# Kernel optimization log

Measured on AMD Instinct MI355X. Metric: run time of the kernel, lower is better.

## Reference

```python
import jax, jax.numpy as jnp
import numpy as np

N, C, H, K = 50000, 256, 8, 16
M = N * K
HID = 4 * C
HD = C // H
SCALE = HD ** -0.5
EPS = 1e-5


def setup_inputs() -> dict:
    key = jax.random.key(0)
    ks = jax.random.split(key, 8)
    init = lambda k, shape, fan: jax.random.normal(k, shape, jnp.float32) * (fan ** -0.5)
    return {
        "feats": jax.random.normal(ks[0], (N, C), jnp.float32),
        "polar_pos": jax.random.normal(ks[1], (N, 3), jnp.float32),
        "edge_index": jax.random.randint(ks[2], (2, M), 0, N, dtype=jnp.int64),
        "ln1_g": jnp.ones((C,), jnp.float32), "ln1_b": jnp.zeros((C,), jnp.float32),
        "qkv_w": init(ks[3], (3 * C, C), C), "qkv_b": jnp.zeros((3 * C,), jnp.float32),
        "proj_w": init(ks[4], (C, C), C), "proj_b": jnp.zeros((C,), jnp.float32),
        "ln2_g": jnp.ones((C,), jnp.float32), "ln2_b": jnp.zeros((C,), jnp.float32),
        "fc1_w": init(ks[5], (HID, C), C), "fc1_b": jnp.zeros((HID,), jnp.float32),
        "fc2_w": init(ks[6], (C, HID), HID), "fc2_b": jnp.zeros((C,), jnp.float32),
    }


def _ln(x, g, b):
    m = x.mean(-1, keepdims=True)
    v = jnp.var(x, axis=-1, keepdims=True)
    return (x - m) * jax.lax.rsqrt(v + EPS) * g + b


def reference(feats, polar_pos, edge_index, ln1_g, ln1_b, qkv_w, qkv_b,
              proj_w, proj_b, ln2_g, ln2_b, fc1_w, fc1_b, fc2_w, fc2_b):
    skip = feats
    x = _ln(feats, ln1_g, ln1_b)

    # edge bookkeeping: sort edges by destination (index_0), matching torch.sort
    idx0 = edge_index[0]
    idx1 = edge_index[1]
    order = jnp.argsort(idx0)  # stable sort
    idx0 = idx0[order]
    idx1 = idx1[order]

    # qkv projection -> (N, 3, H, HD)
    qkv = (x @ qkv_w.T + qkv_b).reshape(N, 3, H, HD)
    q = qkv[:, 0] * SCALE  # (N, H, HD)
    k = qkv[:, 1]
    v = qkv[:, 2]

    # attention_step1_v2: per-edge dot products, (M, H)
    attn = jnp.einsum('mhd,mhd->mh', q[idx0], k[idx1])

    # scatter_softmax over edges grouped by idx0
    mx = jax.ops.segment_max(attn, idx0, num_segments=N)
    e = jnp.exp(attn - mx[idx0])
    s = jax.ops.segment_sum(e, idx0, num_segments=N)
    w = e / s[idx0]  # (M, H)

    # attention_step2: weighted aggregation of neighbor values
    out = jax.ops.segment_sum(w[:, :, None] * v[idx1], idx0, num_segments=N)
    out = out.reshape(N, C)

    out = out @ proj_w.T + proj_b
    feats = skip + out

    y = _ln(feats, ln2_g, ln2_b)
    y = jax.nn.gelu(y @ fc1_w.T + fc1_b, approximate=False)
    y = y @ fc2_w.T + fc2_b
    return feats + y
```

## Files before the change

kernel.cpp:

```cpp
#include <hip/hip_runtime.h>
#include <hip/hip_bf16.h>
#include <cmath>


#define N_NODES 50000
#define C_DIM 256
#define M_EDGES 800000
#define ATT_SCALE 0.17677669529663687f
#define LN_EPS 1e-5f
#define LOG2E 1.4426950408889634f
#define NEG_BIG -3.0e38f

typedef unsigned int uint_t;
typedef unsigned short ushort_t;
typedef short short8 __attribute__((ext_vector_type(8)));
typedef float floatx4 __attribute__((ext_vector_type(4)));

__device__ __forceinline__ ushort_t f2bf(float f) {
  uint_t u = __float_as_uint(f);
  return (ushort_t)((u + 0x7FFFu + ((u >> 16) & 1u)) >> 16);
}
__device__ __forceinline__ float bf_even(uint_t u) { return __uint_as_float(u << 16); }
__device__ __forceinline__ float bf_odd(uint_t u) { return __uint_as_float(u & 0xFFFF0000u); }

__device__ __forceinline__ float gelu_tanh(float x) {
  const float u = 0.7978845608028654f * (x + 0.044715f * x * x * x);
  const float e = __expf(2.0f * u);
  const float t = 1.0f - 2.0f / (e + 1.0f);
  return 0.5f * x * (1.0f + t);
}

__device__ __forceinline__ void gload16(const void* g, void* l) {
  __builtin_amdgcn_global_load_lds(
      (const __attribute__((address_space(1))) void*)g,
      (__attribute__((address_space(3))) void*)l, 16, 0, 0);
}

__global__ __launch_bounds__(256) void ln_kernel(const float* __restrict__ x,
    const float* __restrict__ g, const float* __restrict__ b,
    ushort_t* __restrict__ y)
{
  __shared__ float red[8];
  const int n = blockIdx.x;
  const int t = threadIdx.x;
  float v = x[(size_t)n * C_DIM + t];
  float s = v, s2 = v * v;
#pragma unroll
  for (int m = 1; m < 64; m <<= 1) {
    s += __shfl_xor(s, m);
    s2 += __shfl_xor(s2, m);
  }
  const int wave = t >> 6;
  if ((t & 63) == 0) { red[wave] = s; red[4 + wave] = s2; }
  __syncthreads();
  s = red[0] + red[1] + red[2] + red[3];
  s2 = red[4] + red[5] + red[6] + red[7];
  const float mean = s * (1.0f / 256.0f);
  const float var = fmaxf(s2 * (1.0f / 256.0f) - mean * mean, 0.0f);
  const float r = rsqrtf(var + LN_EPS);
  y[(size_t)n * C_DIM + t] = f2bf((v - mean) * r * g[t] + b[t]);
}

__global__ void cvt_kernel(const float* __restrict__ s0, const float* __restrict__ s1,
                           const float* __restrict__ s2, const float* __restrict__ s3,
                           ushort_t* __restrict__ dst)
{
  const int i = blockIdx.x * 256 + threadIdx.x;
  float v;
  if (i < 196608) v = s0[i];
  else if (i < 262144) v = s1[i - 196608];
  else if (i < 524288) v = s2[i - 262144];
  else v = s3[i - 524288];
  dst[i] = f2bf(v);
}

template <int EPI>
__global__ __launch_bounds__(256, 2) void mfma_gemm(
    const ushort_t* __restrict__ A, const ushort_t* __restrict__ W,
    const float* __restrict__ bias, const float* __restrict__ extra,
    void* __restrict__ OutV, int Kdim, int Jdim)
{
  __shared__ __align__(16) char smem[36864];
  ushort_t* As = (ushort_t*)smem;
  ushort_t* Bs = As + 128 * 64;
  const int t = threadIdx.x;
  const int lane = t & 63;
  const int w = t >> 6;
  const int wm = w & 1;
  const int wn = w >> 1;
  const int rowbase = blockIdx.y * 128;
  const int colbase = blockIdx.x * 128;

  floatx4 acc[4][4] = {};

  int rA[4], kcg[4];
#pragma unroll
  for (int h = 0; h < 4; ++h) {
    const int cidx = h * 256 + w * 64 + lane;
    const int r = cidx >> 3;
    rA[h] = r;
    kcg[h] = (cidx & 7) ^ (r & 7);
  }

  const int rl = lane & 15;
  const int qd = lane >> 4;

  for (int k0 = 0; k0 < Kdim; k0 += 64) {
#pragma unroll
    for (int h = 0; h < 4; ++h) {
      const int r = rA[h];
      int grow = rowbase + r;
      if (grow > N_NODES - 1) grow = N_NODES - 1;
      const int gcol = colbase + r;
      ushort_t* lbase_a = As + (size_t)(h * 256 + w * 64) * 8;
      ushort_t* lbase_b = Bs + (size_t)(h * 256 + w * 64) * 8;
      gload16(A + (size_t)grow * Kdim + k0 + kcg[h] * 8, lbase_a);
      gload16(W + (size_t)gcol * Kdim + k0 + kcg[h] * 8, lbase_b);
    }
    __syncthreads();

#pragma unroll
    for (int h = 0; h < 2; ++h) {
      short8 af[4], bf[4];
#pragma unroll
      for (int tm = 0; tm < 4; ++tm) {
        const int ra = wm * 64 + tm * 16 + rl;
        const int kc = (h * 4 + qd) ^ (ra & 7);
        af[tm] = *(const short8*)(As + ra * 64 + kc * 8);
      }
#pragma unroll
      for (int tn = 0; tn < 4; ++tn) {
        const int rb = wn * 64 + tn * 16 + rl;
        const int kc = (h * 4 + qd) ^ (rb & 7);
        bf[tn] = *(const short8*)(Bs + rb * 64 + kc * 8);
      }
#pragma unroll
      for (int tm = 0; tm < 4; ++tm)
#pragma unroll
        for (int tn = 0; tn < 4; ++tn)
          acc[tm][tn] = __builtin_amdgcn_mfma_f32_16x16x32_bf16(
              af[tm], bf[tn], acc[tm][tn], 0, 0, 0);
    }
    __syncthreads();
  }

  const int q8 = lane >> 3;
  const int c8 = lane & 7;
  if (EPI == 1) {
    float* sc = (float*)smem + w * (64 * 36);
#pragma unroll
    for (int p = 0; p < 2; ++p) {
      __syncthreads();
#pragma unroll
      for (int th = 0; th < 2; ++th) {
        const int tn = p * 2 + th;
#pragma unroll
        for (int tm = 0; tm < 4; ++tm)
#pragma unroll
          for (int r = 0; r < 4; ++r)
            sc[(tm * 16 + qd * 4 + r) * 36 + th * 16 + rl] = acc[tm][tn][r];
      }
      __syncthreads();
      const int col0 = colbase + wn * 64 + p * 32 + c8 * 4;
      const float4 b4 = *(const float4*)(bias + col0);
#pragma unroll
      for (int it = 0; it < 8; ++it) {
        const int lr = it * 8 + q8;
        const int grow = rowbase + wm * 64 + lr;
        if (grow >= N_NODES) continue;
        float4 v = *(const float4*)(sc + lr * 36 + c8 * 4);
        const float4 e4 = *(const float4*)(extra + (size_t)grow * Jdim + col0);
        v.x += b4.x + e4.x; v.y += b4.y + e4.y;
        v.z += b4.z + e4.z; v.w += b4.w + e4.w;
        *(float4*)((float*)OutV + (size_t)grow * Jdim + col0) = v;
      }
    }
  } else {
    ushort_t* su = (ushort_t*)smem + w * (64 * 72);
#pragma unroll
    for (int tn = 0; tn < 4; ++tn) {
      const int col = colbase + wn * 64 + tn * 16 + rl;
      const float bv = bias[col];
#pragma unroll
      for (int tm = 0; tm < 4; ++tm)
#pragma unroll
        for (int r = 0; r < 4; ++r) {
          float v = acc[tm][tn][r] + bv;
          if (EPI == 0) {
            if (col < 256) v *= ATT_SCALE;
          } else {
            v = gelu_tanh(v);
          }
          su[(tm * 16 + qd * 4 + r) * 72 + tn * 16 + rl] = f2bf(v);
        }
    }
    __syncthreads();
#pragma unroll
    for (int it = 0; it < 8; ++it) {
      const int lr = it * 8 + q8;
      const int grow = rowbase + wm * 64 + lr;
      if (grow >= N_NODES) continue;
      const uint4 v = *(const uint4*)(su + lr * 72 + c8 * 8);
      *(uint4*)((ushort_t*)OutV + (size_t)grow * Jdim + colbase + wn * 64 + c8 * 8) = v;
    }
  }
}

__global__ void hist_kernel(const int* __restrict__ idx0, int* __restrict__ counts)
{
  const int m = blockIdx.x * 256 + threadIdx.x;
  if (m < M_EDGES) atomicAdd(&counts[idx0[m]], 1);
}

__global__ __launch_bounds__(256) void scan1_kernel(const int* __restrict__ counts,
    int* __restrict__ offsets, int* __restrict__ bsums)
{
  __shared__ int tmp[256];
  const int t = threadIdx.x;
  const int i = blockIdx.x * 256 + t;
  const int v = (i < N_NODES) ? counts[i] : 0;
  int x = v;
  tmp[t] = x;
  __syncthreads();
#pragma unroll
  for (int off = 1; off < 256; off <<= 1) {
    const int a = (t >= off) ? tmp[t - off] : 0;
    __syncthreads();
    x += a;
    tmp[t] = x;
    __syncthreads();
  }
  if (i < N_NODES) offsets[i] = x - v;
  if (t == 255) bsums[blockIdx.x] = x;
}

__global__ __launch_bounds__(256) void scan2_kernel(int* __restrict__ bsums, int nb)
{
  __shared__ int tmp[256];
  const int t = threadIdx.x;
  const int v = (t < nb) ? bsums[t] : 0;
  int x = v;
  tmp[t] = x;
  __syncthreads();
#pragma unroll
  for (int off = 1; off < 256; off <<= 1) {
    const int a = (t >= off) ? tmp[t - off] : 0;
    __syncthreads();
    x += a;
    tmp[t] = x;
    __syncthreads();
  }
  if (t < nb) bsums[t] = x - v;
}

__global__ void scan3_kernel(int* __restrict__ offsets, const int* __restrict__ bsums)
{
  const int i = blockIdx.x * 256 + threadIdx.x;
  if (i < N_NODES) offsets[i] += bsums[blockIdx.x];
  if (i == 0) offsets[N_NODES] = M_EDGES;
}

__global__ void scatter_kernel(const int* __restrict__ idx0,
    const int* __restrict__ idx1, const int* __restrict__ offsets,
    int* __restrict__ cursor, int* __restrict__ srcs)
{
  const int m = blockIdx.x * 256 + threadIdx.x;
  if (m < M_EDGES) {
    const int n = idx0[m];
    const int p = offsets[n] + atomicAdd(&cursor[n], 1);
    srcs[p] = idx1[m];
  }
}

__global__ __launch_bounds__(256) void attn_kernel(
    const ushort_t* __restrict__ QKVh, const int* __restrict__ offsets,
    const int* __restrict__ srcs, ushort_t* __restrict__ AO)
{
  const int node = blockIdx.x * 4 + (threadIdx.x >> 6);
  if (node >= N_NODES) return;
  const int lane = threadIdx.x & 63;
  const int h = lane & 7;
  const int slot = lane >> 3;
  const int start = offsets[node];
  const int end = offsets[node + 1];

  float q[32];
  {
    const uint4* qr = (const uint4*)(QKVh + (size_t)node * 768 + h * 32);
#pragma unroll
    for (int i = 0; i < 4; ++i) {
      const uint4 u = qr[i];
      q[i * 8 + 0] = bf_even(u.x); q[i * 8 + 1] = bf_odd(u.x);
      q[i * 8 + 2] = bf_even(u.y); q[i * 8 + 3] = bf_odd(u.y);
      q[i * 8 + 4] = bf_even(u.z); q[i * 8 + 5] = bf_odd(u.z);
      q[i * 8 + 6] = bf_even(u.w); q[i * 8 + 7] = bf_odd(u.w);
    }
  }

  float m = NEG_BIG, s = 0.f;
  float o[32];
#pragma unroll
  for (int d = 0; d < 32; ++d) o[d] = 0.f;

  for (int e = start + slot; e < end; e += 8) {
    const int sidx = srcs[e];
    const uint4* kr = (const uint4*)(QKVh + (size_t)sidx * 768 + 256 + h * 32);
    float d = 0.f;
#pragma unroll
    for (int i = 0; i < 4; ++i) {
      const uint4 u = kr[i];
      d += q[i * 8 + 0] * bf_even(u.x) + q[i * 8 + 1] * bf_odd(u.x);
      d += q[i * 8 + 2] * bf_even(u.y) + q[i * 8 + 3] * bf_odd(u.y);
      d += q[i * 8 + 4] * bf_even(u.z) + q[i * 8 + 5] * bf_odd(u.z);
      d += q[i * 8 + 6] * bf_even(u.w) + q[i * 8 + 7] * bf_odd(u.w);
    }
    const float l = d * LOG2E;
    const float mn = fmaxf(m, l);
    const float fac = exp2f(m - mn);
    const float wgt = exp2f(l - mn);
    m = mn;
    s = s * fac + wgt;
    const uint4* vr = (const uint4*)(QKVh + (size_t)sidx * 768 + 512 + h * 32);
#pragma unroll
    for (int i = 0; i < 4; ++i) {
      const uint4 u = vr[i];
      o[i * 8 + 0] = o[i * 8 + 0] * fac + wgt * bf_even(u.x);
      o[i * 8 + 1] = o[i * 8 + 1] * fac + wgt * bf_odd(u.x);
      o[i * 8 + 2] = o[i * 8 + 2] * fac + wgt * bf_even(u.y);
      o[i * 8 + 3] = o[i * 8 + 3] * fac + wgt * bf_odd(u.y);
      o[i * 8 + 4] = o[i * 8 + 4] * fac + wgt * bf_even(u.z);
      o[i * 8 + 5] = o[i * 8 + 5] * fac + wgt * bf_odd(u.z);
      o[i * 8 + 6] = o[i * 8 + 6] * fac + wgt * bf_even(u.w);
      o[i * 8 + 7] = o[i * 8 + 7] * fac + wgt * bf_odd(u.w);
    }
  }

  float mx = m;
  mx = fmaxf(mx, __shfl_xor(mx, 8));
  mx = fmaxf(mx, __shfl_xor(mx, 16));
  mx = fmaxf(mx, __shfl_xor(mx, 32));
  const float fac = exp2f(m - mx);
  s *= fac;
#pragma unroll
  for (int d = 0; d < 32; ++d) o[d] *= fac;

  s += __shfl_xor(s, 8);
  s += __shfl_xor(s, 16);
  s += __shfl_xor(s, 32);

  {
    const bool up = (slot & 4) != 0;
#pragma unroll
    for (int i = 0; i < 16; ++i) {
      const float send = up ? o[i] : o[i + 16];
      const float recv = __shfl_xor(send, 32);
      o[i] = (up ? o[i + 16] : o[i]) + recv;
    }
  }
  {
    const bool up = (slot & 2) != 0;
#pragma unroll
    for (int i = 0; i < 8; ++i) {
      const float send = up ? o[i] : o[i + 8];
      const float recv = __shfl_xor(send, 16);
      o[i] = (up ? o[i + 8] : o[i]) + recv;
    }
  }
  {
    const bool up = (slot & 1) != 0;
#pragma unroll
    for (int i = 0; i < 4; ++i) {
      const float send = up ? o[i] : o[i + 4];
      const float recv = __shfl_xor(send, 8);
      o[i] = (up ? o[i + 4] : o[i]) + recv;
    }
  }
  const int dbase = ((slot & 4) ? 16 : 0) + ((slot & 2) ? 8 : 0) +
                    ((slot & 1) ? 4 : 0);
  const float inv = (end > start) ? 1.0f / s : 0.0f;
  ushort4 st;
  st.x = f2bf(o[0] * inv); st.y = f2bf(o[1] * inv);
  st.z = f2bf(o[2] * inv); st.w = f2bf(o[3] * inv);
  *(ushort4*)(AO + (size_t)node * 256 + h * 32 + dbase) = st;
}

extern "C" void kernel_launch(void* const* d_in, const int* in_sizes, int n_in,
                              void* d_out, int out_size, void* d_ws,
                              size_t ws_size, hipStream_t stream)
{
  const float* feats  = (const float*)d_in[0];
  const int*   edge   = (const int*)d_in[2];
  const float* ln1_g  = (const float*)d_in[3];
  const float* ln1_b  = (const float*)d_in[4];
  const float* qkv_w  = (const float*)d_in[5];
  const float* qkv_b  = (const float*)d_in[6];
  const float* proj_w = (const float*)d_in[7];
  const float* proj_b = (const float*)d_in[8];
  const float* ln2_g  = (const float*)d_in[9];
  const float* ln2_b  = (const float*)d_in[10];
  const float* fc1_w  = (const float*)d_in[11];
  const float* fc1_b  = (const float*)d_in[12];
  const float* fc2_w  = (const float*)d_in[13];
  const float* fc2_b  = (const float*)d_in[14];
  float* out = (float*)d_out;

  ushort_t* Xb   = (ushort_t*)d_ws;
  ushort_t* QKVh = Xb + (size_t)N_NODES * 256;
  ushort_t* AOb  = QKVh + (size_t)N_NODES * 768;
  ushort_t* Hb   = QKVh;
  ushort_t* wb   = AOb + (size_t)N_NODES * 256;
  ushort_t* qkv_wb  = wb;
  ushort_t* proj_wb = qkv_wb + 768 * 256;
  ushort_t* fc1_wb  = proj_wb + 256 * 256;
  ushort_t* fc2_wb  = fc1_wb + 1024 * 256;
  int* counts  = (int*)(fc2_wb + 256 * 1024);
  int* cursor  = counts + N_NODES;
  int* offsets = cursor + N_NODES;
  int* srcs    = offsets + N_NODES + 1;
  int* bsums   = srcs + M_EDGES;
  const size_t required = (size_t)((char*)(bsums + 256) - (char*)d_ws);
  if (ws_size < required) {
    hipMemsetAsync(d_out, 0, (size_t)out_size * sizeof(float), stream);
    return;
  }
  const int* idx0 = edge;
  const int* idx1 = edge + M_EDGES;
  const int rowTiles = (N_NODES + 127) / 128;
  const int scanBlocks = (N_NODES + 255) / 256;

  hipMemsetAsync(counts, 0, 2 * N_NODES * sizeof(int), stream);
  cvt_kernel<<<786432 / 256, 256, 0, stream>>>(qkv_w, proj_w, fc1_w, fc2_w, wb);

  ln_kernel<<<N_NODES, 256, 0, stream>>>(feats, ln1_g, ln1_b, Xb);
  mfma_gemm<0><<<dim3(768 / 128, rowTiles), 256, 0, stream>>>(
      Xb, qkv_wb, qkv_b, nullptr, QKVh, 256, 768);
  hist_kernel<<<(M_EDGES + 255) / 256, 256, 0, stream>>>(idx0, counts);
  scan1_kernel<<<scanBlocks, 256, 0, stream>>>(counts, offsets, bsums);
  scan2_kernel<<<1, 256, 0, stream>>>(bsums, scanBlocks);
  scan3_kernel<<<scanBlocks, 256, 0, stream>>>(offsets, bsums);
  scatter_kernel<<<(M_EDGES + 255) / 256, 256, 0, stream>>>(idx0, idx1, offsets,
                                                            cursor, srcs);
  attn_kernel<<<N_NODES / 4, 256, 0, stream>>>(QKVh, offsets, srcs, AOb);
  mfma_gemm<1><<<dim3(256 / 128, rowTiles), 256, 0, stream>>>(
      AOb, proj_wb, proj_b, feats, out, 256, 256);
  ln_kernel<<<N_NODES, 256, 0, stream>>>(out, ln2_g, ln2_b, Xb);
  mfma_gemm<2><<<dim3(1024 / 128, rowTiles), 256, 0, stream>>>(
      Xb, fc1_wb, fc1_b, nullptr, Hb, 256, 1024);
  mfma_gemm<1><<<dim3(256 / 128, rowTiles), 256, 0, stream>>>(
      Hb, fc2_wb, fc2_b, out, out, 1024, 256);
}
```

Measured before the change: 564.5 us.

## Drop online-softmax max tracking and unify GEMM epilogue for higher occupancy

The edge-attention kernel no longer tracks a running maximum. It accumulates exp(score) and weighted values directly, which removes the per-edge rescale of the 32 output accumulators and the cross-lane max reduction. The GEMM epilogue now stages results through a smaller per-wave float buffer in two row-halves with padded stride 33. That cuts shared memory to 32 KB, drops block-wide syncs, and raises the launch-bounds occupancy hint from 2 to 4. The trade-off is that unstabilized exp can overflow if attention logits grow large, and the tighter register budget may cause spills in the MFMA loop.

```diff
diff --git a/kernel.cpp b/kernel.cpp
--- a/kernel.cpp
+++ b/kernel.cpp
@@ -9,7 +9,6 @@
 #define ATT_SCALE 0.17677669529663687f
 #define LN_EPS 1e-5f
 #define LOG2E 1.4426950408889634f
-#define NEG_BIG -3.0e38f
 
 typedef unsigned int uint_t;
 typedef unsigned short ushort_t;
@@ -75,12 +74,12 @@
 }
 
 template <int EPI>
-__global__ __launch_bounds__(256, 2) void mfma_gemm(
+__global__ __launch_bounds__(256, 4) void mfma_gemm(
     const ushort_t* __restrict__ A, const ushort_t* __restrict__ W,
     const float* __restrict__ bias, const float* __restrict__ extra,
     void* __restrict__ OutV, int Kdim, int Jdim)
 {
-  __shared__ __align__(16) char smem[36864];
+  __shared__ __align__(16) char smem[32768];
   ushort_t* As = (ushort_t*)smem;
   ushort_t* Bs = As + 128 * 64;
   const int t = threadIdx.x;
@@ -146,62 +145,46 @@
 
   const int q8 = lane >> 3;
   const int c8 = lane & 7;
-  if (EPI == 1) {
-    float* sc = (float*)smem + w * (64 * 36);
+  float* sc = (float*)smem + w * 1056;
+  const float qscale = (EPI == 0 && colbase < 256) ? ATT_SCALE : 1.0f;
+#pragma unroll
+  for (int rh = 0; rh < 2; ++rh) {
 #pragma unroll
     for (int p = 0; p < 2; ++p) {
-      __syncthreads();
-#pragma unroll
-      for (int th = 0; th < 2; ++th) {
-        const int tn = p * 2 + th;
-#pragma unroll
-        for (int tm = 0; tm < 4; ++tm)
+#pragma unroll
+      for (int tm2 = 0; tm2 < 2; ++tm2)
+#pragma unroll
+        for (int th = 0; th < 2; ++th)
 #pragma unroll
           for (int r = 0; r < 4; ++r)
-            sc[(tm * 16 + qd * 4 + r) * 36 + th * 16 + rl] = acc[tm][tn][r];
-      }
-      __syncthreads();
+            sc[(tm2 * 16 + qd * 4 + r) * 33 + th * 16 + rl] =
+                acc[rh * 2 + tm2][p * 2 + th][r];
       const int col0 = colbase + wn * 64 + p * 32 + c8 * 4;
       const float4 b4 = *(const float4*)(bias + col0);
 #pragma unroll
-      for (int it = 0; it < 8; ++it) {
+      for (int it = 0; it < 4; ++it) {
         const int lr = it * 8 + q8;
-        const int grow = rowbase + wm * 64 + lr;
+        const int grow = rowbase + wm * 64 + rh * 32 + lr;
         if (grow >= N_NODES) continue;
-        float4 v = *(const float4*)(sc + lr * 36 + c8 * 4);
-        const float4 e4 = *(const float4*)(extra + (size_t)grow * Jdim + col0);
-        v.x += b4.x + e4.x; v.y += b4.y + e4.y;
-        v.z += b4.z + e4.z; v.w += b4.w + e4.w;
-        *(float4*)((float*)OutV + (size_t)grow * Jdim + col0) = v;
+        float4 v = *(const float4*)(sc + lr * 33 + c8 * 4);
+        v.x += b4.x; v.y += b4.y; v.z += b4.z; v.w += b4.w;
+        if (EPI == 1) {
+          const float4 e4 = *(const float4*)(extra + (size_t)grow * Jdim + col0);
+          v.x += e4.x; v.y += e4.y; v.z += e4.z; v.w += e4.w;
+          *(float4*)((float*)OutV + (size_t)grow * Jdim + col0) = v;
+        } else {
+          if (EPI == 0) {
+            v.x *= qscale; v.y *= qscale; v.z *= qscale; v.w *= qscale;
+          } else {
+            v.x = gelu_tanh(v.x); v.y = gelu_tanh(v.y);
+            v.z = gelu_tanh(v.z); v.w = gelu_tanh(v.w);
+          }
+          ushort4 st;
+          st.x = f2bf(v.x); st.y = f2bf(v.y);
+          st.z = f2bf(v.z); st.w = f2bf(v.w);
+          *(ushort4*)((ushort_t*)OutV + (size_t)grow * Jdim + col0) = st;
+        }
       }
-    }
-  } else {
-    ushort_t* su = (ushort_t*)smem + w * (64 * 72);
-#pragma unroll
-    for (int tn = 0; tn < 4; ++tn) {
-      const int col = colbase + wn * 64 + tn * 16 + rl;
-      const float bv = bias[col];
-#pragma unroll
-      for (int tm = 0; tm < 4; ++tm)
-#pragma unroll
-        for (int r = 0; r < 4; ++r) {
-          float v = acc[tm][tn][r] + bv;
-          if (EPI == 0) {
-            if (col < 256) v *= ATT_SCALE;
-          } else {
-            v = gelu_tanh(v);
-          }
-          su[(tm * 16 + qd * 4 + r) * 72 + tn * 16 + rl] = f2bf(v);
-        }
-    }
-    __syncthreads();
-#pragma unroll
-    for (int it = 0; it < 8; ++it) {
-      const int lr = it * 8 + q8;
-      const int grow = rowbase + wm * 64 + lr;
-      if (grow >= N_NODES) continue;
-      const uint4 v = *(const uint4*)(su + lr * 72 + c8 * 8);
-      *(uint4*)((ushort_t*)OutV + (size_t)grow * Jdim + colbase + wn * 64 + c8 * 8) = v;
     }
   }
 }
@@ -297,7 +280,7 @@
     }
   }
 
-  float m = NEG_BIG, s = 0.f;
+  float s = 0.f;
   float o[32];
 #pragma unroll
   for (int d = 0; d < 32; ++d) o[d] = 0.f;
@@ -305,6 +288,7 @@
   for (int e = start + slot; e < end; e += 8) {
     const int sidx = srcs[e];
     const uint4* kr = (const uint4*)(QKVh + (size_t)sidx * 768 + 256 + h * 32);
+    const uint4* vr = (const uint4*)(QKVh + (size_t)sidx * 768 + 512 + h * 32);
     float d = 0.f;
 #pragma unroll
     for (int i = 0; i < 4; ++i) {
@@ -314,35 +298,17 @@
       d += q[i * 8 + 4] * bf_even(u.z) + q[i * 8 + 5] * bf_odd(u.z);
       d += q[i * 8 + 6] * bf_even(u.w) + q[i * 8 + 7] * bf_odd(u.w);
     }
-    const float l = d * LOG2E;
-    const float mn = fmaxf(m, l);
-    const float fac = exp2f(m - mn);
-    const float wgt = exp2f(l - mn);
-    m = mn;
-    s = s * fac + wgt;
-    const uint4* vr = (const uint4*)(QKVh + (size_t)sidx * 768 + 512 + h * 32);
+    const float wgt = exp2f(d * LOG2E);
+    s += wgt;
 #pragma unroll
     for (int i = 0; i < 4; ++i) {
       const uint4 u = vr[i];
-      o[i * 8 + 0] = o[i * 8 + 0] * fac + wgt * bf_even(u.x);
-      o[i * 8 + 1] = o[i * 8 + 1] * fac + wgt * bf_odd(u.x);
-      o[i * 8 + 2] = o[i * 8 + 2] * fac + wgt * bf_even(u.y);
-      o[i * 8 + 3] = o[i * 8 + 3] * fac + wgt * bf_odd(u.y);
-      o[i * 8 + 4] = o[i * 8 + 4] * fac + wgt * bf_even(u.z);
-      o[i * 8 + 5] = o[i * 8 + 5] * fac + wgt * bf_odd(u.z);
-      o[i * 8 + 6] = o[i * 8 + 6] * fac + wgt * bf_even(u.w);
-      o[i * 8 + 7] = o[i * 8 + 7] * fac + wgt * bf_odd(u.w);
-    }
-  }
-
-  float mx = m;
-  mx = fmaxf(mx, __shfl_xor(mx, 8));
-  mx = fmaxf(mx, __shfl_xor(mx, 16));
-  mx = fmaxf(mx, __shfl_xor(mx, 32));
-  const float fac = exp2f(m - mx);
-  s *= fac;
-#pragma unroll
-  for (int d = 0; d < 32; ++d) o[d] *= fac;
+      o[i * 8 + 0] += wgt * bf_even(u.x); o[i * 8 + 1] += wgt * bf_odd(u.x);
+      o[i * 8 + 2] += wgt * bf_even(u.y); o[i * 8 + 3] += wgt * bf_odd(u.y);
+      o[i * 8 + 4] += wgt * bf_even(u.z); o[i * 8 + 5] += wgt * bf_odd(u.z);
+      o[i * 8 + 6] += wgt * bf_even(u.w); o[i * 8 + 7] += wgt * bf_odd(u.w);
+    }
+  }
 
   s += __shfl_xor(s, 8);
   s += __shfl_xor(s, 16);
```

New measurement: 570.7 us. No clear change (+1.1%).
